# Optimization experiments

Measured on AMD Instinct MI355X. Metric: run time of the kernel, lower is better.

Reference implementation:

```python
import jax, jax.numpy as jnp
import numpy as np

BIAS = 1.0
SIGMA = 0.5
EPS = 1e-5


def _mrf_loss(gen, tar):
    # gen, tar: [N, C, H, W]
    N, C, H, W = tar.shape
    meanT = jnp.mean(tar, axis=1, keepdims=True)
    g = gen - meanT
    t = tar - meanT
    g = g / jnp.linalg.norm(g, ord=2, axis=1, keepdims=True)
    t = t / jnp.linalg.norm(t, ord=2, axis=1, keepdims=True)
    # 1x1-patch conv2d with target patches as filters == per-pixel cosine
    # correlation matrix: [N, P=H*W (target positions), H, W (gen positions)]
    tp = t.reshape(N, C, H * W)
    cd = jnp.einsum('nchw,ncp->nphw', g, tp)
    cd = -(cd - 1.0) / 2.0  # cosine distance in [0, 1]
    div = jnp.min(cd, axis=1, keepdims=True)
    rel = cd / (div + EPS)
    e = jnp.exp((BIAS - rel) / SIGMA)
    cs = e / jnp.sum(e, axis=1, keepdims=True)  # sum-normalize over P
    k_max_nc = jnp.max(cs.reshape(N, H * W, -1), axis=2)  # max over gen HW
    div_mrf = jnp.mean(k_max_nc, axis=1)
    return jnp.sum(-jnp.log(div_mrf))


def setup_inputs() -> dict:
    key = jax.random.key(0)
    k1, k2, k3, k4 = jax.random.split(key, 4)
    return {
        'gen3': jax.random.normal(k1, (4, 256, 56, 56), dtype=jnp.float32),
        'tar3': jax.random.normal(k2, (4, 256, 56, 56), dtype=jnp.float32),
        'gen4': jax.random.normal(k3, (4, 512, 28, 28), dtype=jnp.float32),
        'tar4': jax.random.normal(k4, (4, 512, 28, 28), dtype=jnp.float32),
    }


def reference(gen3, tar3, gen4, tar4):
    # weights = [0, 0, 0.5, 1, 0] over VGG relu1..relu5 features
    return 0.5 * _mrf_loss(gen3, tar3) + 1.0 * _mrf_loss(gen4, tar4)
```

## Files before the change

kernel.cpp:

```cpp
#include <hip/hip_runtime.h>
#include <math.h>

typedef __bf16 bf16x8 __attribute__((ext_vector_type(8)));
typedef float f32x4 __attribute__((ext_vector_type(4)));

#define EPSV 1e-5f
#define GLB(p) ((__attribute__((address_space(1))) void*)(p))
#define LDS(p) ((__attribute__((address_space(3))) void*)(p))

__device__ __forceinline__ unsigned fkey(float f) {
  unsigned b = __float_as_uint(f);
  return (b & 0x80000000u) ? ~b : (b | 0x80000000u);
}
__device__ __forceinline__ float funkey(unsigned k) {
  return __uint_as_float((k & 0x80000000u) ? (k & 0x7fffffffu) : ~k);
}

__global__ __launch_bounds__(256) void norm_kernel(
    const float* __restrict__ g3, const float* __restrict__ t3,
    __bf16* __restrict__ G3, __bf16* __restrict__ T3,
    const float* __restrict__ g4, const float* __restrict__ t4,
    __bf16* __restrict__ G4, __bf16* __restrict__ T4)
{
  int lay = blockIdx.z >> 2, n = blockIdx.z & 3;
  const float *gen, *tar; __bf16 *Gh, *Th; int C, P, Ppad, PT, NWORK, NTOT, NG;
  if (lay == 0) { gen = g3; tar = t3; Gh = G3; Th = T3; C = 256; P = 3136; Ppad = 3200; PT = 32; NWORK = 98; NTOT = 100; NG = 8; }
  else          { gen = g4; tar = t4; Gh = G4; Th = T4; C = 512; P = 784;  Ppad = 896;  PT = 16; NWORK = 49; NTOT = 56;  NG = 16; }
  if (blockIdx.y >= (unsigned)NTOT) return;
  int pl, cg;
  if (lay == 0) { pl = threadIdx.x & 31; cg = threadIdx.x >> 5; }
  else          { pl = threadIdx.x & 15; cg = threadIdx.x >> 4; }
  int c0 = cg * 32;

  if (blockIdx.y >= (unsigned)NWORK) {
    int p = P + (blockIdx.y - NWORK) * PT + pl;
    if (p < Ppad) {
      __bf16* tp = Th + ((size_t)n * Ppad + p) * C + c0;
      __bf16* gp = Gh + ((size_t)n * Ppad + p) * C + c0;
      bf16x8 z;
      for (int j = 0; j < 8; j++) z[j] = (__bf16)0.f;
      for (int j = 0; j < 32; j += 8) { *(bf16x8*)(tp + j) = z; *(bf16x8*)(gp + j) = z; }
    }
    return;
  }

  int p = blockIdx.y * PT + pl;
  const float* tb = tar + (size_t)n * C * P + (size_t)c0 * P + p;
  const float* gb = gen + (size_t)n * C * P + (size_t)c0 * P + p;
  float tv[32], gv[32];
  float st = 0.f, sst = 0.f, sg = 0.f, ssg = 0.f;
#pragma unroll
  for (int j = 0; j < 32; j++) {
    tv[j] = tb[(size_t)j * P];
    gv[j] = gb[(size_t)j * P];
  }
#pragma unroll
  for (int j = 0; j < 32; j++) {
    st += tv[j]; sst += tv[j] * tv[j];
    sg += gv[j]; ssg += gv[j] * gv[j];
  }
  __shared__ f32x4 red[16][32];
  red[cg][pl] = f32x4{st, sst, sg, ssg};
  __syncthreads();
  for (int h = NG >> 1; h > 0; h >>= 1) {
    if (cg < h) {
      f32x4 a = red[cg][pl], b = red[cg + h][pl];
      red[cg][pl] = f32x4{a[0] + b[0], a[1] + b[1], a[2] + b[2], a[3] + b[3]};
    }
    __syncthreads();
  }
  f32x4 s = red[0][pl];
  float m = s[0] / (float)C;
  float vt = s[1] - s[0] * s[0] / (float)C;
  float vg = s[3] - 2.f * m * s[2] + (float)C * m * m;
  float it = rsqrtf(fmaxf(vt, 1e-30f));
  float ig = rsqrtf(fmaxf(vg, 1e-30f));
  __bf16* tp = Th + ((size_t)n * Ppad + p) * C + c0;
  __bf16* gp = Gh + ((size_t)n * Ppad + p) * C + c0;
#pragma unroll
  for (int j0 = 0; j0 < 32; j0 += 8) {
    bf16x8 to, go;
    for (int j = 0; j < 8; j++) {
      to[j] = (__bf16)((tv[j0 + j] - m) * it);
      go[j] = (__bf16)((gv[j0 + j] - m) * ig);
    }
    *(bf16x8*)(tp + j0) = to;
    *(bf16x8*)(gp + j0) = go;
  }
}

__global__ __launch_bounds__(256) void gemm_kernel(
    const __bf16* __restrict__ A3, const __bf16* __restrict__ B3,
    __bf16* __restrict__ So3, unsigned* __restrict__ dk3,
    const __bf16* __restrict__ A4, const __bf16* __restrict__ B4,
    __bf16* __restrict__ So4, unsigned* __restrict__ dk4)
{
  __shared__ __attribute__((aligned(16))) __bf16 As[2][4096];
  __shared__ __attribute__((aligned(16))) __bf16 Bs[2][4096];
  int lay = blockIdx.z >> 2, n = blockIdx.z & 3;
  const __bf16 *A, *B; __bf16* S; unsigned* dk; int C, Ppad, Qpad, Preal, NT;
  if (lay == 0) { A = A3; B = B3; S = So3; dk = dk3; C = 256; Ppad = 3200; Qpad = 3200; Preal = 3136; NT = 25; }
  else          { A = A4; B = B4; S = So4; dk = dk4; C = 512; Ppad = 896;  Qpad = 896;  Preal = 784;  NT = 7; }
  if (blockIdx.x >= (unsigned)NT || blockIdx.y >= (unsigned)NT) return;
  int p0 = blockIdx.y * 128, q0 = blockIdx.x * 128;
  int tid = threadIdx.x;
  int w = tid >> 6, lane = tid & 63;
  int lm = lane & 15, lq = lane >> 4;
  int wrow = (w >> 1) * 64, wcol = (w & 1) * 64;

  int srow = tid >> 2;
  int scol = (((tid & 3) ^ ((tid >> 3) & 3)) * 8);
  const __bf16* gA = A + ((size_t)n * Ppad + p0 + srow) * C + scol;
  const __bf16* gB = B + ((size_t)n * Qpad + q0 + srow) * C + scol;
  size_t rowoff = (size_t)64 * C;

  int sl = lq ^ ((lm >> 1) & 3);
  int aoff = (wrow + lm) * 64 + sl * 16;
  int boff = (wcol + lm) * 64 + sl * 16;

  f32x4 acc[4][4];
  for (int i = 0; i < 4; i++)
    for (int j = 0; j < 4; j++)
      acc[i][j] = f32x4{0.f, 0.f, 0.f, 0.f};

  char* lA0 = (char*)&As[0][0] + w * 1024;
  char* lB0 = (char*)&Bs[0][0] + w * 1024;

  __builtin_amdgcn_global_load_lds(GLB(gA), LDS(lA0), 16, 0, 0);
  __builtin_amdgcn_global_load_lds(GLB(gA + rowoff), LDS(lA0 + 4096), 16, 0, 0);
  __builtin_amdgcn_global_load_lds(GLB(gB), LDS(lB0), 16, 0, 0);
  __builtin_amdgcn_global_load_lds(GLB(gB + rowoff), LDS(lB0 + 4096), 16, 0, 0);

  int nk = C >> 5;
  for (int it = 0; it < nk; it++) {
    __syncthreads();
    if (it + 1 < nk) {
      int k0 = (it + 1) << 5;
      char* a = lA0 + ((it + 1) & 1) * 8192;
      char* b = lB0 + ((it + 1) & 1) * 8192;
      __builtin_amdgcn_global_load_lds(GLB(gA + k0), LDS(a), 16, 0, 0);
      __builtin_amdgcn_global_load_lds(GLB(gA + rowoff + k0), LDS(a + 4096), 16, 0, 0);
      __builtin_amdgcn_global_load_lds(GLB(gB + k0), LDS(b), 16, 0, 0);
      __builtin_amdgcn_global_load_lds(GLB(gB + rowoff + k0), LDS(b + 4096), 16, 0, 0);
    }
    const char* ab = (const char*)&As[0][0] + (it & 1) * 8192;
    const char* bb = (const char*)&Bs[0][0] + (it & 1) * 8192;
    bf16x8 af[4], bf[4];
    for (int i = 0; i < 4; i++) af[i] = *(const bf16x8*)(ab + aoff + i * 1024);
    for (int j = 0; j < 4; j++) bf[j] = *(const bf16x8*)(bb + boff + j * 1024);
    for (int i = 0; i < 4; i++)
      for (int j = 0; j < 4; j++)
        acc[i][j] = __builtin_amdgcn_mfma_f32_16x16x32_bf16(af[i], bf[j], acc[i][j], 0, 0, 0);
  }

  __bf16* Sb = S + (size_t)n * Ppad * Qpad;
  float cm[4] = {-INFINITY, -INFINITY, -INFINITY, -INFINITY};
  for (int i = 0; i < 4; i++) {
    for (int j = 0; j < 4; j++) {
      for (int ri = 0; ri < 4; ri++) {
        int pr = p0 + wrow + i * 16 + lq * 4 + ri;
        int qc = q0 + wcol + j * 16 + lm;
        __bf16 bv = (__bf16)acc[i][j][ri];
        Sb[(size_t)pr * Qpad + qc] = bv;
        if (pr < Preal) cm[j] = fmaxf(cm[j], (float)bv);
      }
    }
  }
  for (int j = 0; j < 4; j++) {
    float v = cm[j];
    v = fmaxf(v, __shfl_xor(v, 16, 64));
    v = fmaxf(v, __shfl_xor(v, 32, 64));
    if (lq == 0 && v > -INFINITY) {
      int qc = q0 + wcol + j * 16 + lm;
      atomicMax(&dk[(size_t)n * Qpad + qc], fkey(v));
    }
  }
}

__global__ __launch_bounds__(256) void z_kernel(
    const __bf16* __restrict__ S3, const unsigned* __restrict__ dk3, float* __restrict__ Zp3,
    const __bf16* __restrict__ S4, const unsigned* __restrict__ dk4, float* __restrict__ Zp4)
{
  int lay = blockIdx.z >> 2, n = blockIdx.z & 3;
  const __bf16* S; const unsigned* dk; float* Zp;
  int Ppad, Qreal, Qpad, NSL, SLAB, NX;
  if (lay == 0) { S = S3; dk = dk3; Zp = Zp3; Ppad = 3200; Qreal = 3136; Qpad = 3200; NSL = 98; SLAB = 32; NX = 2; }
  else          { S = S4; dk = dk4; Zp = Zp4; Ppad = 896;  Qreal = 784;  Qpad = 896;  NSL = 49; SLAB = 16; NX = 1; }
  if (blockIdx.x >= (unsigned)NX || blockIdx.y >= (unsigned)NSL) return;
  int q = (blockIdx.x * 256 + threadIdx.x) * 8;
  if (q >= Qreal) return;
  float id[8], nid[8];
  const unsigned* dkp = dk + (size_t)n * Qpad + q;
#pragma unroll
  for (int j = 0; j < 8; j++) {
    float mx = funkey(dkp[j]);
    float d = 0.5f * (1.f - mx) + EPSV;
    id[j] = 1.f / d;
    nid[j] = -id[j];
  }
  int p0 = blockIdx.y * SLAB;
  const __bf16* Sp = S + (size_t)n * Ppad * Qpad + q;
  float acc[8] = {0.f, 0.f, 0.f, 0.f, 0.f, 0.f, 0.f, 0.f};
  for (int pb = 0; pb < SLAB; pb += 8) {
    bf16x8 sv[8];
#pragma unroll
    for (int r = 0; r < 8; r++)
      sv[r] = *(const bf16x8*)(Sp + (size_t)(p0 + pb + r) * Qpad);
#pragma unroll
    for (int r = 0; r < 8; r++)
      for (int j = 0; j < 8; j++)
        acc[j] += __expf(fmaf((float)sv[r][j], id[j], nid[j]));
  }
  float* zp = Zp + ((size_t)n * NSL + blockIdx.y) * Qpad + q;
  *(f32x4*)zp = f32x4{acc[0], acc[1], acc[2], acc[3]};
  *(f32x4*)(zp + 4) = f32x4{acc[4], acc[5], acc[6], acc[7]};
}

__global__ __launch_bounds__(256) void reduce_kernel(
    const float* __restrict__ Zp3, const unsigned* __restrict__ dk3,
    float* __restrict__ invd3, float* __restrict__ c3,
    const float* __restrict__ Zp4, const unsigned* __restrict__ dk4,
    float* __restrict__ invd4, float* __restrict__ c4)
{
  int lay = blockIdx.y >> 2, n = blockIdx.y & 3;
  const float* Zp; const unsigned* dk; float *invd, *c; int Qreal, Qpad, NSL;
  if (lay == 0) { Zp = Zp3; dk = dk3; invd = invd3; c = c3; Qreal = 3136; Qpad = 3200; NSL = 98; }
  else          { Zp = Zp4; dk = dk4; invd = invd4; c = c4; Qreal = 784;  Qpad = 896;  NSL = 49; }
  int q = blockIdx.x * 256 + threadIdx.x;
  if (q >= Qreal) return;
  float s = 0.f;
  for (int sl = 0; sl < NSL; sl++)
    s += Zp[((size_t)n * NSL + sl) * Qpad + q];
  float mx = funkey(dk[(size_t)n * Qpad + q]);
  float d = 0.5f * (1.f - mx) + EPSV;
  float idv = 1.f / d;
  invd[(size_t)n * Qpad + q] = idv;
  c[(size_t)n * Qpad + q] = -logf(s) - idv;
}

__global__ __launch_bounds__(256) void rowmax_kernel(
    const __bf16* __restrict__ S3, const float* __restrict__ invd3,
    const float* __restrict__ c3, float* __restrict__ km3,
    const __bf16* __restrict__ S4, const float* __restrict__ invd4,
    const float* __restrict__ c4, float* __restrict__ km4)
{
  int lay = blockIdx.y >> 2, n = blockIdx.y & 3;
  const __bf16* S; const float *invd, *cc; float* kmax;
  int Qreal, Qpad, Ppad, NB;
  if (lay == 0) { S = S3; invd = invd3; cc = c3; kmax = km3; Qreal = 3136; Qpad = 3200; Ppad = 3200; NB = 784; }
  else          { S = S4; invd = invd4; cc = c4; kmax = km4; Qreal = 784;  Qpad = 896;  Ppad = 896;  NB = 196; }
  if (blockIdx.x >= (unsigned)NB) return;
  int p0 = blockIdx.x * 4;
  const __bf16* Sp = S + ((size_t)n * Ppad + p0) * Qpad;
  const float* id = invd + (size_t)n * Qpad;
  const float* cp = cc + (size_t)n * Qpad;
  int nq8 = Qreal >> 3;
  float m[4] = {-INFINITY, -INFINITY, -INFINITY, -INFINITY};
  for (int i = threadIdx.x; i < nq8; i += 256) {
    f32x4 i0 = *(const f32x4*)(id + (size_t)i * 8);
    f32x4 i1 = *(const f32x4*)(id + (size_t)i * 8 + 4);
    f32x4 c0 = *(const f32x4*)(cp + (size_t)i * 8);
    f32x4 c1 = *(const f32x4*)(cp + (size_t)i * 8 + 4);
    for (int r = 0; r < 4; r++) {
      bf16x8 sv = *(const bf16x8*)(Sp + (size_t)r * Qpad + (size_t)i * 8);
      for (int j = 0; j < 4; j++)
        m[r] = fmaxf(m[r], fmaf((float)sv[j], i0[j], c0[j]));
      for (int j = 0; j < 4; j++)
        m[r] = fmaxf(m[r], fmaf((float)sv[j + 4], i1[j], c1[j]));
    }
  }
  for (int r = 0; r < 4; r++)
    for (int off = 32; off > 0; off >>= 1)
      m[r] = fmaxf(m[r], __shfl_xor(m[r], off, 64));
  __shared__ f32x4 red[4];
  int w = threadIdx.x >> 6;
  if ((threadIdx.x & 63) == 0) red[w] = f32x4{m[0], m[1], m[2], m[3]};
  __syncthreads();
  if (threadIdx.x == 0) {
    for (int r = 0; r < 4; r++) {
      float mr = fmaxf(fmaxf(red[0][r], red[1][r]), fmaxf(red[2][r], red[3][r]));
      kmax[(size_t)n * Ppad + p0 + r] = __expf(mr);
    }
  }
}

__global__ void final_kernel(const float* __restrict__ kmax3, const float* __restrict__ kmax4,
                             float* __restrict__ out)
{
  __shared__ float red[256];
  int tid = threadIdx.x;
  float total = 0.f;
  for (int l = 0; l < 2; l++) {
    const float* km = l ? kmax4 : kmax3;
    int P = l ? 784 : 3136;
    int Ppad = l ? 896 : 3200;
    float wgt = l ? 1.0f : 0.5f;
    for (int n = 0; n < 4; n++) {
      float s = 0.f;
      for (int i = tid; i < P; i += 256) s += km[(size_t)n * Ppad + i];
      red[tid] = s;
      __syncthreads();
      for (int st = 128; st > 0; st >>= 1) {
        if (tid < st) red[tid] += red[tid + st];
        __syncthreads();
      }
      if (tid == 0) total += wgt * (-logf(red[0] / (float)P));
      __syncthreads();
    }
  }
  if (tid == 0) out[0] = total;
}

extern "C" void kernel_launch(void* const* d_in, const int* in_sizes, int n_in,
                              void* d_out, int out_size, void* d_ws, size_t ws_size,
                              hipStream_t stream)
{
  const float* gen3 = (const float*)d_in[0];
  const float* tar3 = (const float*)d_in[1];
  const float* gen4 = (const float*)d_in[2];
  const float* tar4 = (const float*)d_in[3];

  char* ws = (char*)d_ws;
  size_t off = 0;
  auto take = [&](size_t bytes) { char* p = ws + off; off += bytes; return p; };

  unsigned* divkey3 = (unsigned*)take(51200);
  unsigned* divkey4 = (unsigned*)take(14336);
  size_t zero_bytes = off;
  __bf16* That3 = (__bf16*)take(6553600);
  __bf16* Ghat3 = (__bf16*)take(6553600);
  __bf16* That4 = (__bf16*)take(3670016);
  __bf16* Ghat4 = (__bf16*)take(3670016);
  __bf16* S3    = (__bf16*)take(81920000);
  __bf16* S4    = (__bf16*)take(6422528);
  float*  Zp3   = (float*) take(5017600);
  float*  Zp4   = (float*) take(702464);
  float* invd3  = (float*)take(51200);
  float* c3     = (float*)take(51200);
  float* kmax3  = (float*)take(51200);
  float* invd4  = (float*)take(14336);
  float* c4     = (float*)take(14336);
  float* kmax4  = (float*)take(14336);

  hipMemsetAsync(divkey3, 0, zero_bytes, stream);

  norm_kernel<<<dim3(1, 100, 8), 256, 0, stream>>>(gen3, tar3, Ghat3, That3,
                                                   gen4, tar4, Ghat4, That4);
  gemm_kernel<<<dim3(25, 25, 8), 256, 0, stream>>>(That3, Ghat3, S3, divkey3,
                                                   That4, Ghat4, S4, divkey4);
  z_kernel<<<dim3(2, 98, 8), 256, 0, stream>>>(S3, divkey3, Zp3,
                                               S4, divkey4, Zp4);
  reduce_kernel<<<dim3(13, 8), 256, 0, stream>>>(Zp3, divkey3, invd3, c3,
                                                 Zp4, divkey4, invd4, c4);
  rowmax_kernel<<<dim3(784, 8), 256, 0, stream>>>(S3, invd3, c3, kmax3,
                                                  S4, invd4, c4, kmax4);
  final_kernel<<<1, 256, 0, stream>>>(kmax3, kmax4, (float*)d_out);
}
```

Before: 224.6 us.

## Deepen GEMM LDS pipeline to four stages, widen rowmax rows, split reduce accumulators

```diff
diff --git a/kernel.cpp b/kernel.cpp
--- a/kernel.cpp
+++ b/kernel.cpp
@@ -95,8 +95,8 @@
     const __bf16* __restrict__ A4, const __bf16* __restrict__ B4,
     __bf16* __restrict__ So4, unsigned* __restrict__ dk4)
 {
-  __shared__ __attribute__((aligned(16))) __bf16 As[2][4096];
-  __shared__ __attribute__((aligned(16))) __bf16 Bs[2][4096];
+  __shared__ __attribute__((aligned(16))) __bf16 As[4][4096];
+  __shared__ __attribute__((aligned(16))) __bf16 Bs[4][4096];
   int lay = blockIdx.z >> 2, n = blockIdx.z & 3;
   const __bf16 *A, *B; __bf16* S; unsigned* dk; int C, Ppad, Qpad, Preal, NT;
   if (lay == 0) { A = A3; B = B3; S = So3; dk = dk3; C = 256; Ppad = 3200; Qpad = 3200; Preal = 3136; NT = 25; }
@@ -113,6 +113,8 @@
   const __bf16* gA = A + ((size_t)n * Ppad + p0 + srow) * C + scol;
   const __bf16* gB = B + ((size_t)n * Qpad + q0 + srow) * C + scol;
   size_t rowoff = (size_t)64 * C;
+  char* lAbase = (char*)&As[0][0] + w * 1024;
+  char* lBbase = (char*)&Bs[0][0] + w * 1024;
 
   int sl = lq ^ ((lm >> 1) & 3);
   int aoff = (wrow + lm) * 64 + sl * 16;
@@ -123,35 +125,40 @@
     for (int j = 0; j < 4; j++)
       acc[i][j] = f32x4{0.f, 0.f, 0.f, 0.f};
 
-  char* lA0 = (char*)&As[0][0] + w * 1024;
-  char* lB0 = (char*)&Bs[0][0] + w * 1024;
-
-  __builtin_amdgcn_global_load_lds(GLB(gA), LDS(lA0), 16, 0, 0);
-  __builtin_amdgcn_global_load_lds(GLB(gA + rowoff), LDS(lA0 + 4096), 16, 0, 0);
-  __builtin_amdgcn_global_load_lds(GLB(gB), LDS(lB0), 16, 0, 0);
-  __builtin_amdgcn_global_load_lds(GLB(gB + rowoff), LDS(lB0 + 4096), 16, 0, 0);
-
-  int nk = C >> 5;
-  for (int it = 0; it < nk; it++) {
-    __syncthreads();
-    if (it + 1 < nk) {
-      int k0 = (it + 1) << 5;
-      char* a = lA0 + ((it + 1) & 1) * 8192;
-      char* b = lB0 + ((it + 1) & 1) * 8192;
-      __builtin_amdgcn_global_load_lds(GLB(gA + k0), LDS(a), 16, 0, 0);
-      __builtin_amdgcn_global_load_lds(GLB(gA + rowoff + k0), LDS(a + 4096), 16, 0, 0);
-      __builtin_amdgcn_global_load_lds(GLB(gB + k0), LDS(b), 16, 0, 0);
-      __builtin_amdgcn_global_load_lds(GLB(gB + rowoff + k0), LDS(b + 4096), 16, 0, 0);
-    }
-    const char* ab = (const char*)&As[0][0] + (it & 1) * 8192;
-    const char* bb = (const char*)&Bs[0][0] + (it & 1) * 8192;
+  auto issue = [&](int s) {
+    int k0 = s << 5;
+    char* a = lAbase + (s & 3) * 8192;
+    char* b = lBbase + (s & 3) * 8192;
+    __builtin_amdgcn_global_load_lds(GLB(gA + k0), LDS(a), 16, 0, 0);
+    __builtin_amdgcn_global_load_lds(GLB(gA + rowoff + k0), LDS(a + 4096), 16, 0, 0);
+    __builtin_amdgcn_global_load_lds(GLB(gB + k0), LDS(b), 16, 0, 0);
+    __builtin_amdgcn_global_load_lds(GLB(gB + rowoff + k0), LDS(b + 4096), 16, 0, 0);
+  };
+  auto compute = [&](int it) {
+    const char* ab = (const char*)&As[0][0] + (it & 3) * 8192;
+    const char* bb = (const char*)&Bs[0][0] + (it & 3) * 8192;
     bf16x8 af[4], bf[4];
     for (int i = 0; i < 4; i++) af[i] = *(const bf16x8*)(ab + aoff + i * 1024);
     for (int j = 0; j < 4; j++) bf[j] = *(const bf16x8*)(bb + boff + j * 1024);
     for (int i = 0; i < 4; i++)
       for (int j = 0; j < 4; j++)
         acc[i][j] = __builtin_amdgcn_mfma_f32_16x16x32_bf16(af[i], bf[j], acc[i][j], 0, 0, 0);
-  }
+  };
+
+  int nk = C >> 5;
+  issue(0); issue(1); issue(2);
+  for (int it = 0; it < nk - 2; it++) {
+    asm volatile("s_waitcnt vmcnt(8)" ::: "memory");
+    __builtin_amdgcn_s_barrier();
+    compute(it);
+    if (it + 3 < nk) issue(it + 3);
+  }
+  asm volatile("s_waitcnt vmcnt(4)" ::: "memory");
+  __builtin_amdgcn_s_barrier();
+  compute(nk - 2);
+  asm volatile("s_waitcnt vmcnt(0)" ::: "memory");
+  __builtin_amdgcn_s_barrier();
+  compute(nk - 1);
 
   __bf16* Sb = S + (size_t)n * Ppad * Qpad;
   float cm[4] = {-INFINITY, -INFINITY, -INFINITY, -INFINITY};
@@ -228,9 +235,16 @@
   else          { Zp = Zp4; dk = dk4; invd = invd4; c = c4; Qreal = 784;  Qpad = 896;  NSL = 49; }
   int q = blockIdx.x * 256 + threadIdx.x;
   if (q >= Qreal) return;
-  float s = 0.f;
-  for (int sl = 0; sl < NSL; sl++)
-    s += Zp[((size_t)n * NSL + sl) * Qpad + q];
+  float s0 = 0.f, s1 = 0.f, s2 = 0.f, s3 = 0.f;
+  int sl = 0;
+  for (; sl + 4 <= NSL; sl += 4) {
+    s0 += Zp[((size_t)n * NSL + sl) * Qpad + q];
+    s1 += Zp[((size_t)n * NSL + sl + 1) * Qpad + q];
+    s2 += Zp[((size_t)n * NSL + sl + 2) * Qpad + q];
+    s3 += Zp[((size_t)n * NSL + sl + 3) * Qpad + q];
+  }
+  for (; sl < NSL; sl++) s0 += Zp[((size_t)n * NSL + sl) * Qpad + q];
+  float s = (s0 + s1) + (s2 + s3);
   float mx = funkey(dk[(size_t)n * Qpad + q]);
   float d = 0.5f * (1.f - mx) + EPSV;
   float idv = 1.f / d;
@@ -247,21 +261,24 @@
   int lay = blockIdx.y >> 2, n = blockIdx.y & 3;
   const __bf16* S; const float *invd, *cc; float* kmax;
   int Qreal, Qpad, Ppad, NB;
-  if (lay == 0) { S = S3; invd = invd3; cc = c3; kmax = km3; Qreal = 3136; Qpad = 3200; Ppad = 3200; NB = 784; }
-  else          { S = S4; invd = invd4; cc = c4; kmax = km4; Qreal = 784;  Qpad = 896;  Ppad = 896;  NB = 196; }
+  if (lay == 0) { S = S3; invd = invd3; cc = c3; kmax = km3; Qreal = 3136; Qpad = 3200; Ppad = 3200; NB = 392; }
+  else          { S = S4; invd = invd4; cc = c4; kmax = km4; Qreal = 784;  Qpad = 896;  Ppad = 896;  NB = 98; }
   if (blockIdx.x >= (unsigned)NB) return;
-  int p0 = blockIdx.x * 4;
+  int p0 = blockIdx.x * 8;
   const __bf16* Sp = S + ((size_t)n * Ppad + p0) * Qpad;
   const float* id = invd + (size_t)n * Qpad;
   const float* cp = cc + (size_t)n * Qpad;
   int nq8 = Qreal >> 3;
-  float m[4] = {-INFINITY, -INFINITY, -INFINITY, -INFINITY};
+  float m[8];
+#pragma unroll
+  for (int r = 0; r < 8; r++) m[r] = -INFINITY;
   for (int i = threadIdx.x; i < nq8; i += 256) {
     f32x4 i0 = *(const f32x4*)(id + (size_t)i * 8);
     f32x4 i1 = *(const f32x4*)(id + (size_t)i * 8 + 4);
     f32x4 c0 = *(const f32x4*)(cp + (size_t)i * 8);
     f32x4 c1 = *(const f32x4*)(cp + (size_t)i * 8 + 4);
-    for (int r = 0; r < 4; r++) {
+#pragma unroll
+    for (int r = 0; r < 8; r++) {
       bf16x8 sv = *(const bf16x8*)(Sp + (size_t)r * Qpad + (size_t)i * 8);
       for (int j = 0; j < 4; j++)
         m[r] = fmaxf(m[r], fmaf((float)sv[j], i0[j], c0[j]));
@@ -269,18 +286,19 @@
         m[r] = fmaxf(m[r], fmaf((float)sv[j + 4], i1[j], c1[j]));
     }
   }
-  for (int r = 0; r < 4; r++)
+#pragma unroll
+  for (int r = 0; r < 8; r++)
     for (int off = 32; off > 0; off >>= 1)
       m[r] = fmaxf(m[r], __shfl_xor(m[r], off, 64));
-  __shared__ f32x4 red[4];
+  __shared__ float red[4][8];
   int w = threadIdx.x >> 6;
-  if ((threadIdx.x & 63) == 0) red[w] = f32x4{m[0], m[1], m[2], m[3]};
+  if ((threadIdx.x & 63) == 0)
+    for (int r = 0; r < 8; r++) red[w][r] = m[r];
   __syncthreads();
-  if (threadIdx.x == 0) {
-    for (int r = 0; r < 4; r++) {
-      float mr = fmaxf(fmaxf(red[0][r], red[1][r]), fmaxf(red[2][r], red[3][r]));
-      kmax[(size_t)n * Ppad + p0 + r] = __expf(mr);
-    }
+  if (threadIdx.x < 8) {
+    int r = threadIdx.x;
+    float mr = fmaxf(fmaxf(red[0][r], red[1][r]), fmaxf(red[2][r], red[3][r]));
+    kmax[(size_t)n * Ppad + p0 + r] = __expf(mr);
   }
 }
 
@@ -352,7 +370,7 @@
                                                S4, divkey4, Zp4);
   reduce_kernel<<<dim3(13, 8), 256, 0, stream>>>(Zp3, divkey3, invd3, c3,
                                                  Zp4, divkey4, invd4, c4);
-  rowmax_kernel<<<dim3(784, 8), 256, 0, stream>>>(S3, invd3, c3, kmax3,
+  rowmax_kernel<<<dim3(392, 8), 256, 0, stream>>>(S3, invd3, c3, kmax3,
                                                   S4, invd4, c4, kmax4);
   final_kernel<<<1, 256, 0, stream>>>(kmax3, kmax4, (float*)d_out);
 }
```

New measurement: 219.7 us. -2.2%, faster.
